# Kernel tuning notes

Measured on AMD Instinct MI355X. Metric: run time of the kernel, lower is better.

The kernel has to match this reference:

```python
import jax, jax.numpy as jnp
import numpy as np

B, N, NODE_DIM = 32, 512, 2
D, H, L, FF = 512, 8, 3, 2048
DK = D // H  # key/val dim per head = 64
EPS = 1e-5


def batch_norm(h, gamma, beta):
    # BatchNorm1d in training mode over flattened (batch*graph) dim, biased var
    flat = h.reshape(-1, h.shape[-1])
    mu = flat.mean(axis=0)
    var = flat.var(axis=0)
    out = (flat - mu) * jax.lax.rsqrt(var + EPS) * gamma + beta
    return out.reshape(h.shape)


def mha(h, Wq, Wk, Wv, Wo):
    # h: [B,N,D]; Wq/Wk/Wv: [H,D,DK]; Wo: [H,DK,D]
    Q = jnp.einsum('bnd,hdk->hbnk', h, Wq)
    K = jnp.einsum('bnd,hdk->hbnk', h, Wk)
    V = jnp.einsum('bnd,hdk->hbnk', h, Wv)
    scores = jnp.einsum('hbqk,hbnk->hbqn', Q, K) / jnp.sqrt(jnp.float32(DK))
    attn = jax.nn.softmax(scores, axis=-1)
    heads = jnp.einsum('hbqn,hbnk->hbqk', attn, V)
    return jnp.einsum('hbqk,hkd->bqd', heads, Wo)


def setup_inputs() -> dict:
    key = jax.random.key(0)
    ks = jax.random.split(key, 16)
    u = lambda k, shape, fan: jax.random.uniform(k, shape, jnp.float32, -1.0, 1.0) / np.sqrt(fan)
    return {
        'x': jax.random.normal(ks[0], (B, N, NODE_DIM), jnp.float32),
        'We': u(ks[1], (D, NODE_DIM), NODE_DIM),
        'be': u(ks[2], (D,), NODE_DIM),
        'Wq': u(ks[3], (L, H, D, DK), DK),
        'Wk': u(ks[4], (L, H, D, DK), DK),
        'Wv': u(ks[5], (L, H, D, DK), DK),
        'Wo': u(ks[6], (L, H, DK, D), D),
        'g1': jnp.ones((L, D), jnp.float32),
        'b1': jnp.zeros((L, D), jnp.float32),
        'W1': u(ks[7], (L, FF, D), D),
        'bb1': u(ks[8], (L, FF), D),
        'W2': u(ks[9], (L, D, FF), FF),
        'bb2': u(ks[10], (L, D), FF),
        'g2': jnp.ones((L, D), jnp.float32),
        'b2': jnp.zeros((L, D), jnp.float32),
    }


def reference(x, We, be, Wq, Wk, Wv, Wo, g1, b1, W1, bb1, W2, bb2, g2, b2):
    # init embed: Linear(node_dim -> D)
    h = jnp.einsum('bnc,dc->bnd', x, We) + be
    for i in range(L):
        h = batch_norm(h + mha(h, Wq[i], Wk[i], Wv[i], Wo[i]), g1[i], b1[i])
        ff = jax.nn.relu(jnp.einsum('bnd,fd->bnf', h, W1[i]) + bb1[i])
        ff = jnp.einsum('bnf,df->bnd', ff, W2[i]) + bb2[i]
        h = batch_norm(h + ff, g2[i], b2[i])
    return h, h.mean(axis=1)
```

## Files before the change

kernel.cpp:

```cpp
#include <hip/hip_runtime.h>
#include <hip/hip_bf16.h>

#define Bx 32
#define Nx 512
#define Dx 512
#define Hx 8
#define DKx 64
#define FFx 2048
#define TOK (Bx * Nx)
#define EPSx 1e-5f

typedef float  f32x4  __attribute__((ext_vector_type(4)));
typedef _Float16 hfrag8 __attribute__((ext_vector_type(8)));
typedef _Float16 h4     __attribute__((ext_vector_type(4)));
typedef _Float16 h2     __attribute__((ext_vector_type(2)));

struct hf2 { _Float16 hi, lo; };
__device__ __forceinline__ hf2 split2h(float v) {
    _Float16 h = (_Float16)v;
    hf2 r; r.hi = h; r.lo = (_Float16)(v - (float)h);
    return r;
}

__device__ __forceinline__ void gl16(const void* g, void* l) {
    __builtin_amdgcn_global_load_lds(
        (const __attribute__((address_space(1))) unsigned int*)g,
        (__attribute__((address_space(3))) unsigned int*)l, 16, 0, 0);
}

__device__ __forceinline__ int swzoff(int row, int q) {
    int p = row >> 1;
    int sl = ((row & 1) << 2) | q;
    int s = sl ^ (p & 7);
    return p * 128 + s * 16;
}

__device__ __forceinline__ float ldsel(const void* p32, const void* p16, size_t i, int f32) {
    return f32 ? ((const float*)p32)[i]
               : __bfloat162float(((const __hip_bfloat16*)p16)[i]);
}

__global__ void detect_kernel(const void* __restrict__ x, int* __restrict__ flag)
{
    if (threadIdx.x == 0 && blockIdx.x == 0) {
        const unsigned short* u = (const unsigned short*)x;
        int hits = 0;
        for (int i = 0; i < 256; ++i) {
            int e = (u[i] >> 7) & 0xFF;
            if (e >= 0x86) ++hits;
        }
        *flag = (hits > 8) ? 1 : 0;
    }
}

__global__ __launch_bounds__(256) void cvt_kernel(
    const void* __restrict__ W, _Float16* __restrict__ o, const int* __restrict__ dtp)
{
    const int f32 = *dtp;
    size_t idx = (size_t)blockIdx.x * 256 + threadIdx.x;
    o[idx] = (_Float16)ldsel(W, W, idx, f32);
}

__global__ __launch_bounds__(256) void transpose_cvt_kernel(
    const void* __restrict__ W, _Float16* __restrict__ o,
    int R, int C, const int* __restrict__ dtp)
{
    const int f32 = *dtp;
    __shared__ float tile[64][65];
    const size_t mbase = (size_t)blockIdx.z * R * C;
    const int c0 = blockIdx.x * 64, r0 = blockIdx.y * 64;
    const int tc = threadIdx.x & 63, tg = threadIdx.x >> 6;
    #pragma unroll
    for (int i = 0; i < 16; ++i) {
        int r = tg * 16 + i;
        tile[r][tc] = ldsel(W, W, mbase + (size_t)(r0 + r) * C + c0 + tc, f32);
    }
    __syncthreads();
    #pragma unroll
    for (int i = 0; i < 16; ++i) {
        int cc = tg * 16 + i;
        o[mbase + (size_t)(c0 + cc) * R + r0 + tc] = (_Float16)tile[tc][cc];
    }
}

__global__ __launch_bounds__(256) void embed_kernel(
    const void* __restrict__ x, const void* __restrict__ We,
    const void* __restrict__ be, _Float16* __restrict__ hh, _Float16* __restrict__ hl,
    const int* __restrict__ dtp)
{
    const int f32 = *dtp;
    size_t idx = (size_t)blockIdx.x * 256 + threadIdx.x;
    int d = idx & (Dx - 1);
    size_t t = idx >> 9;
    float v = ldsel(x, x, t * 2, f32)     * ldsel(We, We, d * 2, f32) +
              ldsel(x, x, t * 2 + 1, f32) * ldsel(We, We, d * 2 + 1, f32) +
              ldsel(be, be, d, f32);
    hf2 s = split2h(v);
    hh[idx] = s.hi; hl[idx] = s.lo;
}

template <int EPI, int OHF, int STATS, int BM>
__global__ __launch_bounds__(256, BM == 64 ? 4 : 3) void gemm3(
    const _Float16* __restrict__ Ahg, const _Float16* __restrict__ Bg,
    const void* __restrict__ bias32, const void* __restrict__ bias16,
    const _Float16* __restrict__ residH, const _Float16* __restrict__ residL,
    void* __restrict__ outp, float* __restrict__ part,
    int M, int N, int K, const int* __restrict__ dtp)
{
    constexpr int MT   = BM / 32;
    constexpr int APL  = BM * 64;
    constexpr int BUFB = APL + 8192;
    const int f32 = *dtp;
    __shared__ __align__(16) unsigned char lds[3][BUFB];

    const int tid = threadIdx.x;
    const int gx = gridDim.x;
    const int nwg = gx * gridDim.y;
    int flat = blockIdx.y * gx + blockIdx.x;
    flat = (flat & 7) * (nwg >> 3) + (flat >> 3);
    const int bm = (flat / gx) * BM;
    const int bn = (flat % gx) * 128;

    const int lane = tid & 63, wv = tid >> 6;
    const int quad = lane >> 4, lrow = lane & 15;
    const int wm = (wv & 1) * (BM / 2), wn = (wv >> 1) * 64;

    f32x4 acc[MT][4] = {};

    const int s2 = (lane & 7) ^ (lane >> 3);
    const int rl = 2 * (lane >> 3) + (s2 >> 2);
    const int cl = (s2 & 3) * 8;

    const _Float16* wsrc = nullptr;
    int wrb = 0, wbase = 0, wchunks = 0;
    if constexpr (BM == 128) {
        if (wv < 2) {
            wsrc = (wv == 0) ? Ahg : Bg;
            wrb  = (wv == 0) ? bm : bn;
            wbase = wv * 8192;
            wchunks = 8;
        }
    } else {
        if (wv == 0)      { wsrc = Ahg; wrb = bm;      wbase = 0;    wchunks = 4; }
        else if (wv == 1) { wsrc = Bg;  wrb = bn;      wbase = 4096; wchunks = 4; }
        else if (wv == 2) { wsrc = Bg;  wrb = bn + 64; wbase = 8192; wchunks = 4; }
    }

    auto stage = [&](int step) {
        if (wsrc) {
            const int buf = step % 3;
            const int k0 = step << 5;
            const _Float16* s = wsrc + (size_t)(wrb + rl) * K + k0 + cl;
            for (int ch = 0; ch < wchunks; ++ch)
                gl16(s + (size_t)(ch * 16) * K, &lds[buf][wbase + ch * 1024]);
        }
    };

    int offA[MT], offB[4];
    #pragma unroll
    for (int mt = 0; mt < MT; ++mt) offA[mt] = swzoff(wm + mt * 16 + lrow, quad);
    #pragma unroll
    for (int nt = 0; nt < 4; ++nt) offB[nt] = APL + swzoff(wn + nt * 16 + lrow, quad);

    const int NT = K >> 5;
    stage(0);
    stage(1);

    for (int i = 0; i < NT; ++i) {
        if (i + 1 < NT) {
            if constexpr (BM == 128) asm volatile("s_waitcnt vmcnt(8)" ::: "memory");
            else                     asm volatile("s_waitcnt vmcnt(4)" ::: "memory");
        } else {
            asm volatile("s_waitcnt vmcnt(0)" ::: "memory");
        }
        __builtin_amdgcn_sched_barrier(0);
        __builtin_amdgcn_s_barrier();
        __builtin_amdgcn_sched_barrier(0);

        if (i + 2 < NT) stage(i + 2);

        const unsigned char* bp = lds[i % 3];
        hfrag8 ah[MT];
        #pragma unroll
        for (int mt = 0; mt < MT; ++mt)
            ah[mt] = *(const hfrag8*)(bp + offA[mt]);
        #pragma unroll
        for (int nt = 0; nt < 4; ++nt) {
            hfrag8 b = *(const hfrag8*)(bp + offB[nt]);
            #pragma unroll
            for (int mt = 0; mt < MT; ++mt)
                acc[mt][nt] = __builtin_amdgcn_mfma_f32_16x16x32_f16(ah[mt], b, acc[mt][nt], 0, 0, 0);
        }

        __builtin_amdgcn_sched_barrier(0);
        asm volatile("s_waitcnt lgkmcnt(0)" ::: "memory");
        __builtin_amdgcn_sched_barrier(0);
    }

    #pragma unroll
    for (int nt = 0; nt < 4; ++nt) {
        const int n = bn + wn + nt * 16 + lrow;
        float cs = 0.f, cq = 0.f;
        #pragma unroll
        for (int mt = 0; mt < MT; ++mt)
            #pragma unroll
            for (int reg = 0; reg < 4; ++reg) {
                int m = bm + wm + mt * 16 + quad * 4 + reg;
                float v = acc[mt][nt][reg];
                if constexpr (EPI == 1) { v += ldsel(bias32, bias16, n, f32); v = fmaxf(v, 0.f); }
                if constexpr (EPI == 2) {
                    if (bias32) v += ldsel(bias32, bias16, n, f32);
                    size_t ridx = (size_t)m * N + n;
                    v += (float)residH[ridx] + (float)residL[ridx];
                }
                size_t oidx = (size_t)m * N + n;
                if constexpr (OHF == 1) ((_Float16*)outp)[oidx] = (_Float16)v;
                else if constexpr (OHF == 2) {
                    hf2 s = split2h(v);
                    h2 pk; pk[0] = s.hi; pk[1] = s.lo;
                    ((h2*)outp)[oidx] = pk;
                }
                else ((float*)outp)[oidx] = v;
                if constexpr (STATS) { cs += v; cq += v * v; }
            }
        if constexpr (STATS) {
            cs += __shfl_xor(cs, 16); cs += __shfl_xor(cs, 32);
            cq += __shfl_xor(cq, 16); cq += __shfl_xor(cq, 32);
            if (quad == 0) {
                float* pb = part + (size_t)(bm >> 6) * 1024;
                atomicAdd(&pb[n], cs);
                atomicAdd(&pb[512 + n], cq);
            }
        }
    }
}

__global__ __launch_bounds__(256, 3) void qkv_mfma(
    const _Float16* __restrict__ Ahg,
    const _Float16* __restrict__ QT, const _Float16* __restrict__ KT,
    const _Float16* __restrict__ VT,
    _Float16* __restrict__ Qhg, _Float16* __restrict__ Qlg,
    _Float16* __restrict__ Khg, _Float16* __restrict__ Vo, int M, int K)
{
    __shared__ __align__(16) unsigned char lds[3][2 * 8192];

    const int tid = threadIdx.x;
    const int gx = gridDim.x;
    const int nwg = gx * gridDim.y;
    int flat = blockIdx.y * gx + blockIdx.x;
    flat = (flat & 7) * (nwg >> 3) + (flat >> 3);
    const int bm = (flat / gx) * 128;
    const int bn = (flat % gx) * 128;

    const int sel = bn >> 9;
    const int nloc = bn & 511;
    const _Float16* Bg = ((sel == 0) ? QT : (sel == 1) ? KT : VT) + (size_t)nloc * K;

    const int lane = tid & 63, wv = tid >> 6;
    const int quad = lane >> 4, lrow = lane & 15;
    const int wm = (wv & 1) * 64, wn = (wv >> 1) * 64;

    f32x4 acc[4][4] = {};

    const int s2 = (lane & 7) ^ (lane >> 3);
    const int rl = 2 * (lane >> 3) + (s2 >> 2);
    const int cl = (s2 & 3) * 8;

    const bool doStage = (wv < 2);
    const _Float16* wsrc = (wv == 0) ? Ahg : Bg;
    const int wrb = (wv == 0) ? bm : 0;

    auto stage = [&](int step) {
        if (doStage) {
            const int buf = step % 3;
            const int k0 = step << 5;
            const _Float16* s = wsrc + (size_t)(wrb + rl) * K + k0 + cl;
            #pragma unroll
            for (int ch = 0; ch < 8; ++ch)
                gl16(s + (size_t)(ch * 16) * K, &lds[buf][wv * 8192 + ch * 1024]);
        }
    };

    int offA[4], offB[4];
    #pragma unroll
    for (int mt = 0; mt < 4; ++mt) offA[mt] = swzoff(wm + mt * 16 + lrow, quad);
    #pragma unroll
    for (int nt = 0; nt < 4; ++nt) offB[nt] = 8192 + swzoff(wn + nt * 16 + lrow, quad);

    const int NT = K >> 5;
    stage(0);
    stage(1);

    for (int i = 0; i < NT; ++i) {
        if (i + 1 < NT) asm volatile("s_waitcnt vmcnt(8)" ::: "memory");
        else            asm volatile("s_waitcnt vmcnt(0)" ::: "memory");
        __builtin_amdgcn_sched_barrier(0);
        __builtin_amdgcn_s_barrier();
        __builtin_amdgcn_sched_barrier(0);

        if (i + 2 < NT) stage(i + 2);

        const unsigned char* bp = lds[i % 3];
        hfrag8 ah[4];
        #pragma unroll
        for (int mt = 0; mt < 4; ++mt)
            ah[mt] = *(const hfrag8*)(bp + offA[mt]);
        #pragma unroll
        for (int nt = 0; nt < 4; ++nt) {
            hfrag8 b = *(const hfrag8*)(bp + offB[nt]);
            #pragma unroll
            for (int mt = 0; mt < 4; ++mt)
                acc[mt][nt] = __builtin_amdgcn_mfma_f32_16x16x32_f16(ah[mt], b, acc[mt][nt], 0, 0, 0);
        }

        __builtin_amdgcn_sched_barrier(0);
        asm volatile("s_waitcnt lgkmcnt(0)" ::: "memory");
        __builtin_amdgcn_sched_barrier(0);
    }

    const int nb = M >> 9;
    #pragma unroll
    for (int mt = 0; mt < 4; ++mt)
        #pragma unroll
        for (int nt = 0; nt < 4; ++nt) {
            const int ncol = nloc + wn + nt * 16 + lrow;
            const int head = ncol >> 6, dk = ncol & 63;
            const int m0 = bm + wm + mt * 16 + quad * 4;
            const int b_ = m0 >> 9, q = m0 & 511;
            if (sel == 2) {
                h4 v;
                #pragma unroll
                for (int reg = 0; reg < 4; ++reg) v[reg] = (_Float16)acc[mt][nt][reg];
                *(h4*)&Vo[(((size_t)head * nb + b_) * DKx + dk) * Nx + q] = v;
            } else if (sel == 1) {
                #pragma unroll
                for (int reg = 0; reg < 4; ++reg) {
                    size_t oidx = (((size_t)head * nb + b_) * Nx + (q + reg)) * DKx + dk;
                    Khg[oidx] = (_Float16)acc[mt][nt][reg];
                }
            } else {
                #pragma unroll
                for (int reg = 0; reg < 4; ++reg) {
                    hf2 s = split2h(acc[mt][nt][reg]);
                    size_t oidx = (((size_t)head * nb + b_) * Nx + (q + reg)) * DKx + dk;
                    Qhg[oidx] = s.hi;
                    Qlg[oidx] = s.lo;
                }
            }
        }
}

__global__ __launch_bounds__(256, 4) void attn_kernel(
    const _Float16* __restrict__ Qhg, const _Float16* __restrict__ Qlg,
    const _Float16* __restrict__ Khg, const _Float16* __restrict__ Vtg,
    _Float16* __restrict__ heads)
{
    __shared__ __align__(16) _Float16  Kh[64][72];
    __shared__ __align__(16) _Float16  Vt[64][72];
    __shared__ __align__(16) _Float16  Sp[64][72];
    __shared__ float ml[64], ll[64], al[64];

    const int tid = threadIdx.x;
    const int q0 = blockIdx.x * 64;
    const int hb = blockIdx.y;
    const size_t base = (size_t)hb * (Nx * DKx);
    const int lane = tid & 63, wv = tid >> 6;
    const int quad = lane >> 4, lrow = lane & 15;
    const int wm = (wv & 1) * 32, wn = (wv >> 1) * 32;
    const int sr = tid >> 2, sc = (tid & 3) * 16;

    {
        size_t off = base + (size_t)(q0 + sr) * DKx + sc;
        *(hfrag8*)&Kh[sr][sc]     = *(const hfrag8*)(Qhg + off);
        *(hfrag8*)&Kh[sr][sc + 8] = *(const hfrag8*)(Qhg + off + 8);
        *(hfrag8*)&Sp[sr][sc]     = *(const hfrag8*)(Qlg + off);
        *(hfrag8*)&Sp[sr][sc + 8] = *(const hfrag8*)(Qlg + off + 8);
    }
    if (tid < 64) { ml[tid] = -INFINITY; ll[tid] = 0.f; }
    __syncthreads();

    hfrag8 qh[2][2], qlo[2][2];
    #pragma unroll
    for (int mt = 0; mt < 2; ++mt)
        #pragma unroll
        for (int ks = 0; ks < 2; ++ks) {
            qh[mt][ks]  = *(const hfrag8*)&Kh[wm + mt * 16 + lrow][ks * 32 + quad * 8];
            qlo[mt][ks] = *(const hfrag8*)&Sp[wm + mt * 16 + lrow][ks * 32 + quad * 8];
        }
    __syncthreads();

    hfrag8 pkh[2], pv[2];
    auto loadKV = [&](int n0) {
        size_t off = base + (size_t)(n0 + sr) * DKx + sc;
        pkh[0] = *(const hfrag8*)(Khg + off);
        pkh[1] = *(const hfrag8*)(Khg + off + 8);
        const _Float16* vp = Vtg + base + (size_t)sr * Nx + n0 + sc;
        pv[0] = *(const hfrag8*)vp;
        pv[1] = *(const hfrag8*)(vp + 8);
    };
    auto storeKV = [&]() {
        *(hfrag8*)&Kh[sr][sc]     = pkh[0];
        *(hfrag8*)&Kh[sr][sc + 8] = pkh[1];
        *(hfrag8*)&Vt[sr][sc]     = pv[0];
        *(hfrag8*)&Vt[sr][sc + 8] = pv[1];
    };

    f32x4 accO[2][2] = {};

    loadKV(0); storeKV();
    __syncthreads();

    for (int n0 = 0; n0 < Nx; n0 += 64) {
        const bool more = (n0 + 64 < Nx);
        if (more) loadKV(n0 + 64);

        f32x4 accS[2][2] = {};
        __builtin_amdgcn_s_setprio(1);
        #pragma unroll
        for (int ks = 0; ks < 2; ++ks) {
            hfrag8 bh[2];
            #pragma unroll
            for (int nt = 0; nt < 2; ++nt)
                bh[nt] = *(const hfrag8*)&Kh[wn + nt * 16 + lrow][ks * 32 + quad * 8];
            #pragma unroll
            for (int mt = 0; mt < 2; ++mt)
                #pragma unroll
                for (int nt = 0; nt < 2; ++nt) {
                    accS[mt][nt] = __builtin_amdgcn_mfma_f32_16x16x32_f16(qh[mt][ks],  bh[nt], accS[mt][nt], 0, 0, 0);
                    accS[mt][nt] = __builtin_amdgcn_mfma_f32_16x16x32_f16(qlo[mt][ks], bh[nt], accS[mt][nt], 0, 0, 0);
                }
        }
        __builtin_amdgcn_s_setprio(0);
        #pragma unroll
        for (int mt = 0; mt < 2; ++mt)
            #pragma unroll
            for (int nt = 0; nt < 2; ++nt)
                #pragma unroll
                for (int reg = 0; reg < 4; ++reg)
                    Sp[wm + mt * 16 + quad * 4 + reg][wn + nt * 16 + lrow] =
                        (_Float16)(accS[mt][nt][reg] * 0.125f);
        __syncthreads();

        {
            hfrag8 s0 = *(const hfrag8*)&Sp[sr][sc];
            hfrag8 s1 = *(const hfrag8*)&Sp[sr][sc + 8];
            float rmax = -INFINITY;
            #pragma unroll
            for (int j = 0; j < 8; ++j) {
                rmax = fmaxf(rmax, (float)s0[j]);
                rmax = fmaxf(rmax, (float)s1[j]);
            }
            rmax = fmaxf(rmax, __shfl_xor(rmax, 1));
            rmax = fmaxf(rmax, __shfl_xor(rmax, 2));
            float mold = ml[sr];
            float mnew = fmaxf(mold, rmax);
            float sum = 0.f;
            hfrag8 p0, p1;
            #pragma unroll
            for (int j = 0; j < 8; ++j) {
                float pa = __expf((float)s0[j] - mnew);
                float pb = __expf((float)s1[j] - mnew);
                sum += pa + pb;
                p0[j] = (_Float16)pa;
                p1[j] = (_Float16)pb;
            }
            sum += __shfl_xor(sum, 1);
            sum += __shfl_xor(sum, 2);
            *(hfrag8*)&Sp[sr][sc]     = p0;
            *(hfrag8*)&Sp[sr][sc + 8] = p1;
            if ((tid & 3) == 0) {
                float alpha = __expf(mold - mnew);
                ml[sr] = mnew;
                ll[sr] = ll[sr] * alpha + sum;
                al[sr] = alpha;
            }
        }
        __syncthreads();

        #pragma unroll
        for (int mt = 0; mt < 2; ++mt) {
            float a0 = al[wm + mt * 16 + quad * 4 + 0];
            float a1 = al[wm + mt * 16 + quad * 4 + 1];
            float a2 = al[wm + mt * 16 + quad * 4 + 2];
            float a3 = al[wm + mt * 16 + quad * 4 + 3];
            #pragma unroll
            for (int nt = 0; nt < 2; ++nt) {
                accO[mt][nt][0] *= a0; accO[mt][nt][1] *= a1;
                accO[mt][nt][2] *= a2; accO[mt][nt][3] *= a3;
            }
        }
        __builtin_amdgcn_s_setprio(1);
        #pragma unroll
        for (int ks = 0; ks < 2; ++ks) {
            hfrag8 ap[2], bv[2];
            #pragma unroll
            for (int mt = 0; mt < 2; ++mt)
                ap[mt] = *(const hfrag8*)&Sp[wm + mt * 16 + lrow][ks * 32 + quad * 8];
            #pragma unroll
            for (int nt = 0; nt < 2; ++nt)
                bv[nt] = *(const hfrag8*)&Vt[wn + nt * 16 + lrow][ks * 32 + quad * 8];
            #pragma unroll
            for (int mt = 0; mt < 2; ++mt)
                #pragma unroll
                for (int nt = 0; nt < 2; ++nt)
                    accO[mt][nt] = __builtin_amdgcn_mfma_f32_16x16x32_f16(ap[mt], bv[nt], accO[mt][nt], 0, 0, 0);
        }
        __builtin_amdgcn_s_setprio(0);

        if (more) {
            __syncthreads();
            storeKV();
            __syncthreads();
        }
    }

    const int h_ = hb >> 5, b_ = hb & 31;
    #pragma unroll
    for (int mt = 0; mt < 2; ++mt)
        #pragma unroll
        for (int reg = 0; reg < 4; ++reg) {
            int qrow = wm + mt * 16 + quad * 4 + reg;
            float invl = 1.f / ll[qrow];
            size_t tok = (size_t)b_ * Nx + (q0 + qrow);
            #pragma unroll
            for (int nt = 0; nt < 2; ++nt) {
                int dk = wn + nt * 16 + lrow;
                heads[tok * Dx + h_ * DKx + dk] = (_Float16)(accO[mt][nt][reg] * invl);
            }
        }
}

__global__ __launch_bounds__(256) void bn_final(
    const float* __restrict__ part, float* __restrict__ stats)
{
    int c = blockIdx.x * 256 + threadIdx.x;
    float s = 0.f;
    for (int rt = 0; rt < 256; ++rt) s += part[(size_t)rt * 1024 + c];
    stats[c] = s;
}

__global__ __launch_bounds__(256) void bn_norm(
    const h2* __restrict__ tpk, const float* __restrict__ stats,
    const void* __restrict__ g32, const void* __restrict__ g16,
    const void* __restrict__ b32, const void* __restrict__ b16,
    _Float16* __restrict__ hh, _Float16* __restrict__ hl,
    float* __restrict__ out32, const int* __restrict__ dtp)
{
    const int f32 = *dtp;
    size_t idx = (size_t)blockIdx.x * 256 + threadIdx.x;
    int c = idx & (Dx - 1);
    const float invM = 1.f / (float)TOK;
    float mu = stats[c] * invM;
    float var = stats[Dx + c] * invM - mu * mu;
    h2 tv = tpk[idx];
    float t = (float)tv[0] + (float)tv[1];
    float v = (t - mu) * rsqrtf(var + EPSx) * ldsel(g32, g16, c, f32) + ldsel(b32, b16, c, f32);
    hf2 s = split2h(v);
    hh[idx] = s.hi; hl[idx] = s.lo;
    if (out32) out32[idx] = v;
}

__global__ __launch_bounds__(256) void out_mean_part(
    const _Float16* __restrict__ hh, const _Float16* __restrict__ hl, float* __restrict__ part)
{
    int b = blockIdx.x;
    int g = blockIdx.y;
    int d = threadIdx.x;
    float s0 = 0.f, s1 = 0.f;
    for (int n = g * 64; n < g * 64 + 64; ++n) {
        size_t idx = ((size_t)b * Nx + n) * Dx;
        s0 += (float)hh[idx + d]       + (float)hl[idx + d];
        s1 += (float)hh[idx + d + 256] + (float)hl[idx + d + 256];
    }
    part[((size_t)b * 8 + g) * Dx + d]       = s0;
    part[((size_t)b * 8 + g) * Dx + d + 256] = s1;
}

__global__ __launch_bounds__(256) void out_mean_final(
    const float* __restrict__ part, float* __restrict__ out2)
{
    size_t o = (size_t)blockIdx.x * 256 + threadIdx.x;
    int b = (int)(o >> 9), d = (int)(o & 511);
    float s = 0.f;
    #pragma unroll
    for (int g = 0; g < 8; ++g) s += part[((size_t)b * 8 + g) * Dx + d];
    out2[o] = s * (1.f / (float)Nx);
}

extern "C" void kernel_launch(void* const* d_in, const int* in_sizes, int n_in,
                              void* d_out, int out_size, void* d_ws, size_t ws_size,
                              hipStream_t stream)
{
    const void* x   = d_in[0];
    const void* We  = d_in[1];
    const void* be  = d_in[2];
    const void* Wq  = d_in[3];
    const void* Wk  = d_in[4];
    const void* Wv  = d_in[5];
    const void* Wo  = d_in[6];
    const void* g1  = d_in[7];
    const void* b1  = d_in[8];
    const void* W1  = d_in[9];
    const void* bb1 = d_in[10];
    const void* W2  = d_in[11];
    const void* bb2 = d_in[12];
    const void* g2  = d_in[13];
    const void* b2  = d_in[14];

    const size_t szHD = (size_t)TOK * Dx;
    const size_t QKN  = (size_t)Hx * Bx * Nx * DKx;
    const size_t szQT = (size_t)3 * Hx * DKx * Dx;
    const size_t szW1 = (size_t)3 * FFx * Dx;
    const size_t szWqkvL = (size_t)Hx * Dx * DKx;

    h2* tpk        = (h2*)d_ws;
    float* stats   = (float*)(tpk + szHD);
    int*   dtp     = (int*)(stats + 2 * Dx);
    _Float16* hh   = (_Float16*)(stats + 2 * Dx + 64);
    _Float16* hl   = hh + szHD;
    _Float16* region = hl + szHD;

    _Float16* heads = region;
    _Float16* Qhg   = heads + szHD;
    _Float16* Qlg   = Qhg + QKN;
    _Float16* Khg   = Qlg + QKN;
    _Float16* Vtg   = Khg + QKN;
    _Float16* ffbuf = region;

    _Float16* WqT = Vtg + QKN;
    _Float16* WkT = WqT + szQT;
    _Float16* WvT = WkT + szQT;
    _Float16* WoT = WvT + szQT;
    _Float16* W1c = WoT + szQT;
    _Float16* W2c = W1c + szW1;
    float*    part = (float*)(W2c + szW1);

    auto p32 = [](const void* p, size_t e) { return (const void*)((const float*)p + e); };
    auto p16 = [](const void* p, size_t e) { return (const void*)((const __hip_bfloat16*)p + e); };

    detect_kernel<<<1, 64, 0, stream>>>(x, dtp);

    transpose_cvt_kernel<<<dim3(1, 8, 24), 256, 0, stream>>>(Wq, WqT, Dx, DKx, dtp);
    transpose_cvt_kernel<<<dim3(1, 8, 24), 256, 0, stream>>>(Wk, WkT, Dx, DKx, dtp);
    transpose_cvt_kernel<<<dim3(1, 8, 24), 256, 0, stream>>>(Wv, WvT, Dx, DKx, dtp);
    transpose_cvt_kernel<<<dim3(8, 8, 3), 256, 0, stream>>>(Wo, WoT, Dx, Dx, dtp);
    cvt_kernel<<<szW1 / 256, 256, 0, stream>>>(W1, W1c, dtp);
    cvt_kernel<<<szW1 / 256, 256, 0, stream>>>(W2, W2c, dtp);

    embed_kernel<<<TOK * Dx / 256, 256, 0, stream>>>(x, We, be, hh, hl, dtp);

    const dim3 gQKV(12, TOK / 128);
    const dim3 gWo(Dx / 128, TOK / 64);
    const dim3 gAttn(Nx / 64, Hx * Bx);
    const dim3 gFF1(FFx / 128, TOK / 128);
    const dim3 gFF2(Dx / 128, TOK / 64);
    const size_t partBytes = 256 * 1024 * sizeof(float);
    for (int l = 0; l < 3; ++l) {
        const size_t eQ = (size_t)l * szWqkvL;
        const size_t e1 = (size_t)l * FFx * Dx;
        const size_t eD = (size_t)l * Dx, eF = (size_t)l * FFx;
        const bool last = (l == 2);

        qkv_mfma<<<gQKV, 256, 0, stream>>>(
            hh, WqT + eQ, WkT + eQ, WvT + eQ,
            Qhg, Qlg, Khg, Vtg, TOK, Dx);
        attn_kernel<<<gAttn, 256, 0, stream>>>(Qhg, Qlg, Khg, Vtg, heads);

        hipMemsetAsync(part, 0, partBytes, stream);
        gemm3<2, 2, 1, 64><<<gWo, 256, 0, stream>>>(
            heads, WoT + eQ,
            nullptr, nullptr, hh, hl, tpk, part, TOK, Dx, Dx, dtp);
        bn_final<<<4, 256, 0, stream>>>(part, stats);
        bn_norm<<<TOK * Dx / 256, 256, 0, stream>>>(
            tpk, stats, p32(g1, eD), p16(g1, eD), p32(b1, eD), p16(b1, eD),
            hh, hl, nullptr, dtp);

        gemm3<1, 1, 0, 128><<<gFF1, 256, 0, stream>>>(
            hh, W1c + e1,
            p32(bb1, eF), p16(bb1, eF), nullptr, nullptr, ffbuf, nullptr,
            TOK, FFx, Dx, dtp);
        hipMemsetAsync(part, 0, partBytes, stream);
        gemm3<2, 2, 1, 64><<<gFF2, 256, 0, stream>>>(
            ffbuf, W2c + e1,
            p32(bb2, eD), p16(bb2, eD), hh, hl, tpk, part, TOK, Dx, FFx, dtp);
        bn_final<<<4, 256, 0, stream>>>(part, stats);
        bn_norm<<<TOK * Dx / 256, 256, 0, stream>>>(
            tpk, stats, p32(g2, eD), p16(g2, eD), p32(b2, eD), p16(b2, eD),
            hh, hl, last ? (float*)d_out : nullptr, dtp);
    }

    out_mean_part<<<dim3(Bx, 8), 256, 0, stream>>>(hh, hl, part);
    out_mean_final<<<Bx * Dx / 256, 256, 0, stream>>>(part, (float*)d_out + (size_t)TOK * Dx);
}
```

Measured before the change: 1.224 ms.

## Use 128-row tiles and two-k-step pipelined iterations for FF2 GEMM

Adds a KSTEP template parameter to the GEMM. With KSTEP=2 it uses four LDS buffers and processes two 32-wide k-steps per barrier pair, prefetching the next two steps before waiting. The FF2 GEMM (K=2048) switches from 64-row to 128-row tiles with this mode, halving the grid and aiming to cut barrier overhead and improve operand reuse. The trade-off is higher LDS use and lower occupancy (launch bound of 2 waves per SIMD), and the partial-stats reduction now sees fewer, larger blocks.

```diff
diff --git a/kernel.cpp b/kernel.cpp
--- a/kernel.cpp
+++ b/kernel.cpp
@@ -99,8 +99,8 @@
     hh[idx] = s.hi; hl[idx] = s.lo;
 }
 
-template <int EPI, int OHF, int STATS, int BM>
-__global__ __launch_bounds__(256, BM == 64 ? 4 : 3) void gemm3(
+template <int EPI, int OHF, int STATS, int BM, int KSTEP>
+__global__ __launch_bounds__(256, KSTEP == 2 ? 2 : (BM == 64 ? 4 : 3)) void gemm3(
     const _Float16* __restrict__ Ahg, const _Float16* __restrict__ Bg,
     const void* __restrict__ bias32, const void* __restrict__ bias16,
     const _Float16* __restrict__ residH, const _Float16* __restrict__ residL,
@@ -110,8 +110,9 @@
     constexpr int MT   = BM / 32;
     constexpr int APL  = BM * 64;
     constexpr int BUFB = APL + 8192;
+    constexpr int NB   = (KSTEP == 2) ? 4 : 3;
     const int f32 = *dtp;
-    __shared__ __align__(16) unsigned char lds[3][BUFB];
+    __shared__ __align__(16) unsigned char lds[NB][BUFB];
 
     const int tid = threadIdx.x;
     const int gx = gridDim.x;
@@ -148,7 +149,7 @@
 
     auto stage = [&](int step) {
         if (wsrc) {
-            const int buf = step % 3;
+            const int buf = step % NB;
             const int k0 = step << 5;
             const _Float16* s = wsrc + (size_t)(wrb + rl) * K + k0 + cl;
             for (int ch = 0; ch < wchunks; ++ch)
@@ -162,24 +163,8 @@
     #pragma unroll
     for (int nt = 0; nt < 4; ++nt) offB[nt] = APL + swzoff(wn + nt * 16 + lrow, quad);
 
-    const int NT = K >> 5;
-    stage(0);
-    stage(1);
-
-    for (int i = 0; i < NT; ++i) {
-        if (i + 1 < NT) {
-            if constexpr (BM == 128) asm volatile("s_waitcnt vmcnt(8)" ::: "memory");
-            else                     asm volatile("s_waitcnt vmcnt(4)" ::: "memory");
-        } else {
-            asm volatile("s_waitcnt vmcnt(0)" ::: "memory");
-        }
-        __builtin_amdgcn_sched_barrier(0);
-        __builtin_amdgcn_s_barrier();
-        __builtin_amdgcn_sched_barrier(0);
-
-        if (i + 2 < NT) stage(i + 2);
-
-        const unsigned char* bp = lds[i % 3];
+    auto compute = [&](int step) {
+        const unsigned char* bp = lds[step % NB];
         hfrag8 ah[MT];
         #pragma unroll
         for (int mt = 0; mt < MT; ++mt)
@@ -191,10 +176,55 @@
             for (int mt = 0; mt < MT; ++mt)
                 acc[mt][nt] = __builtin_amdgcn_mfma_f32_16x16x32_f16(ah[mt], b, acc[mt][nt], 0, 0, 0);
         }
-
-        __builtin_amdgcn_sched_barrier(0);
-        asm volatile("s_waitcnt lgkmcnt(0)" ::: "memory");
-        __builtin_amdgcn_sched_barrier(0);
+    };
+
+    const int NT = K >> 5;
+
+    if constexpr (KSTEP == 1) {
+        stage(0);
+        stage(1);
+        for (int i = 0; i < NT; ++i) {
+            if (i + 1 < NT) {
+                if constexpr (BM == 128) asm volatile("s_waitcnt vmcnt(8)" ::: "memory");
+                else                     asm volatile("s_waitcnt vmcnt(4)" ::: "memory");
+            } else {
+                asm volatile("s_waitcnt vmcnt(0)" ::: "memory");
+            }
+            __builtin_amdgcn_sched_barrier(0);
+            __builtin_amdgcn_s_barrier();
+            __builtin_amdgcn_sched_barrier(0);
+
+            if (i + 2 < NT) stage(i + 2);
+
+            compute(i);
+
+            __builtin_amdgcn_sched_barrier(0);
+            asm volatile("s_waitcnt lgkmcnt(0)" ::: "memory");
+            __builtin_amdgcn_sched_barrier(0);
+        }
+    } else {
+        const int NI = NT >> 1;
+        stage(0);
+        stage(1);
+        for (int j = 0; j < NI; ++j) {
+            __builtin_amdgcn_s_barrier();
+            __builtin_amdgcn_sched_barrier(0);
+
+            if (2 * j + 2 < NT) { stage(2 * j + 2); stage(2 * j + 3); }
+
+            if (j + 1 < NI) asm volatile("s_waitcnt vmcnt(16)" ::: "memory");
+            else            asm volatile("s_waitcnt vmcnt(0)"  ::: "memory");
+            __builtin_amdgcn_sched_barrier(0);
+            __builtin_amdgcn_s_barrier();
+            __builtin_amdgcn_sched_barrier(0);
+
+            compute(2 * j);
+            compute(2 * j + 1);
+
+            __builtin_amdgcn_sched_barrier(0);
+            asm volatile("s_waitcnt lgkmcnt(0)" ::: "memory");
+            __builtin_amdgcn_sched_barrier(0);
+        }
     }
 
     #pragma unroll
@@ -653,7 +683,7 @@
     const dim3 gWo(Dx / 128, TOK / 64);
     const dim3 gAttn(Nx / 64, Hx * Bx);
     const dim3 gFF1(FFx / 128, TOK / 128);
-    const dim3 gFF2(Dx / 128, TOK / 64);
+    const dim3 gFF2(Dx / 128, TOK / 128);
     const size_t partBytes = 256 * 1024 * sizeof(float);
     for (int l = 0; l < 3; ++l) {
         const size_t eQ = (size_t)l * szWqkvL;
@@ -667,7 +697,7 @@
         attn_kernel<<<gAttn, 256, 0, stream>>>(Qhg, Qlg, Khg, Vtg, heads);
 
         hipMemsetAsync(part, 0, partBytes, stream);
-        gemm3<2, 2, 1, 64><<<gWo, 256, 0, stream>>>(
+        gemm3<2, 2, 1, 64, 1><<<gWo, 256, 0, stream>>>(
             heads, WoT + eQ,
             nullptr, nullptr, hh, hl, tpk, part, TOK, Dx, Dx, dtp);
         bn_final<<<4, 256, 0, stream>>>(part, stats);
@@ -675,12 +705,12 @@
             tpk, stats, p32(g1, eD), p16(g1, eD), p32(b1, eD), p16(b1, eD),
             hh, hl, nullptr, dtp);
 
-        gemm3<1, 1, 0, 128><<<gFF1, 256, 0, stream>>>(
+        gemm3<1, 1, 0, 128, 1><<<gFF1, 256, 0, stream>>>(
             hh, W1c + e1,
             p32(bb1, eF), p16(bb1, eF), nullptr, nullptr, ffbuf, nullptr,
             TOK, FFx, Dx, dtp);
         hipMemsetAsync(part, 0, partBytes, stream);
-        gemm3<2, 2, 1, 64><<<gFF2, 256, 0, stream>>>(
+        gemm3<2, 2, 1, 128, 2><<<gFF2, 256, 0, stream>>>(
             ffbuf, W2c + e1,
             p32(bb2, eD), p16(bb2, eD), hh, hl, tpk, part, TOK, Dx, FFx, dtp);
         bn_final<<<4, 256, 0, stream>>>(part, stats);
```

New measurement: 1.238 ms. About the same (+1.2%).
